# Performance work log

Hardware: AMD Instinct MI355X
Metric: run time of the kernel (lower is better)

## Reference

```python
import jax, jax.numpy as jnp
import numpy as np

B, S, E, D, H = 4, 2048, 512, 64, 8
NEG = float(np.finfo(np.float64).min)  # tf uses tf.float64.min; overflows to -inf in fp32, same softmax effect


def setup_inputs() -> dict:
    key = jax.random.key(0)
    ks = jax.random.split(key, 6)
    std = 0.05  # tf.random_normal_initializer default stddev
    x = jax.random.normal(ks[0], (B, S, E), dtype=jnp.float32)
    Wq = jax.random.normal(ks[1], (H, E, D), dtype=jnp.float32) * std
    Wk = jax.random.normal(ks[2], (H, E, D), dtype=jnp.float32) * std
    Wvd = jax.random.normal(ks[3], (H, E, D), dtype=jnp.float32) * std
    Wvu = jax.random.normal(ks[4], (H, D, E), dtype=jnp.float32) * std
    Wo = jax.random.normal(ks[5], (H, 1), dtype=jnp.float32) * std
    return {"x": x, "Wq": Wq, "Wk": Wk, "Wvd": Wvd, "Wvu": Wvu, "Wo": Wo}


def reference(x, Wq, Wk, Wvd, Wvu, Wo):
    # Per-head projections, vectorized over the head axis h
    Q = jnp.einsum("bse,hed->bhsd", x, Wq)  # [B,H,S,D]
    K = jnp.einsum("bse,hed->bhsd", x, Wk)
    score = jnp.einsum("bhsd,bhtd->bhst", Q, K) / jnp.sqrt(jnp.float32(D))
    # tf.linalg.band_part(score, -1, 0): keep lower triangle (causal)
    tril = jnp.tril(jnp.ones((S, S), dtype=bool))
    score = jnp.where(tril, score, 0.0)
    # tf.where(score != 0, score, float64.min): masks zeros (incl. any exact-zero kept entries)
    score = jnp.where(score != 0, score, jnp.float32(NEG))
    attn = jax.nn.softmax(score, axis=-1)  # [B,H,S,S]
    # low-rank value projection: x @ (Wvdown @ Wvup) per head
    Wv = jnp.einsum("hed,hdf->hef", Wvd, Wvu)  # [H,E,E]
    V = jnp.einsum("bse,hef->bhsf", x, Wv)      # [B,H,S,E]
    heads = jnp.einsum("bhst,bhte->bhse", attn, V)  # [B,H,S,E]
    # stack on last axis then matmul with Wo[H,1] == weighted sum over heads
    out = jnp.einsum("bhse,h->bse", heads, Wo[:, 0])
    return out
```

## Files before the change

kernel.cpp:

```cpp
#include <hip/hip_runtime.h>
#include <math.h>

namespace {
constexpr int B = 4, S = 2048, E = 512, D = 64, H = 8;
constexpr int KD = 512;

typedef short bf8 __attribute__((ext_vector_type(8)));
typedef short bf4 __attribute__((ext_vector_type(4)));
typedef float f4 __attribute__((ext_vector_type(4)));

__device__ __forceinline__ short f2bf(float f) {
  union { float f; unsigned u; } v; v.f = f;
  const unsigned r = v.u + 0x7fffu + ((v.u >> 16) & 1u);
  return (short)(r >> 16);
}

__device__ __forceinline__ unsigned cvt_pk_bf16(float a, float b) {
  unsigned r;
  asm("v_cvt_pk_bf16_f32 %0, %1, %2" : "=v"(r) : "v"(a), "v"(b));
  return r;
}

__device__ __forceinline__ void gload16(const void* g, void* l) {
  __builtin_amdgcn_global_load_lds(
      (const __attribute__((address_space(1))) unsigned int*)g,
      (__attribute__((address_space(3))) unsigned int*)l, 16, 0, 0);
}

__global__ __launch_bounds__(256) void xb_kernel(const float* __restrict__ x,
                                                 short* __restrict__ xb) {
  const size_t i = ((size_t)blockIdx.x * 256 + threadIdx.x) * 8;
  const float4 v0 = *(const float4*)(x + i);
  const float4 v1 = *(const float4*)(x + i + 4);
  bf8 o;
  o[0] = f2bf(v0.x); o[1] = f2bf(v0.y); o[2] = f2bf(v0.z); o[3] = f2bf(v0.w);
  o[4] = f2bf(v1.x); o[5] = f2bf(v1.y); o[6] = f2bf(v1.z); o[7] = f2bf(v1.w);
  *(bf8*)(xb + i) = o;
}

__global__ __launch_bounds__(256) void wcat_kernel(
    const float* __restrict__ Wq, const float* __restrict__ Wk,
    const float* __restrict__ Wvd, short* __restrict__ WcatT) {
  const int cb = blockIdx.x;
  const int e0 = blockIdx.y * 64;
  const int w = cb >> 3, h = cb & 7;
  const float* Wsel = (w == 0) ? Wq : (w == 1) ? Wk : Wvd;
  const float* Wp = Wsel + (size_t)h * E * D;
  __shared__ float T[64][65];
  const int tid = threadIdx.x;
#pragma unroll
  for (int i = 0; i < 4; ++i) {
    const int f = tid + i * 256;
    const int r = f >> 4, c4 = f & 15;
    const float4 v = *(const float4*)(Wp + (size_t)(e0 + r) * D + c4 * 4);
    T[r][c4 * 4 + 0] = v.x; T[r][c4 * 4 + 1] = v.y;
    T[r][c4 * 4 + 2] = v.z; T[r][c4 * 4 + 3] = v.w;
  }
  __syncthreads();
#pragma unroll
  for (int i = 0; i < 4; ++i) {
    const int f = tid + i * 256;
    const int dr = f >> 4, e4 = f & 15;
    bf4 o;
#pragma unroll
    for (int j = 0; j < 4; ++j) o[j] = f2bf(T[e4 * 4 + j][dr]);
    *(bf4*)(WcatT + (size_t)(cb * 64 + dr) * KD + e0 + e4 * 4) = o;
  }
}

__global__ __launch_bounds__(256) void w2t_kernel(
    const float* __restrict__ Wvu, const float* __restrict__ Wo,
    short* __restrict__ W2T) {
  const int h = blockIdx.x;
  const int e0 = blockIdx.y * 64;
  const float wo = Wo[h];
  __shared__ float T[64][65];
  const int tid = threadIdx.x;
#pragma unroll
  for (int i = 0; i < 4; ++i) {
    const int f = tid + i * 256;
    const int r = f >> 4, c4 = f & 15;
    const float4 v = *(const float4*)(Wvu + ((size_t)h * D + r) * E + e0 + c4 * 4);
    T[r][c4 * 4 + 0] = v.x * wo; T[r][c4 * 4 + 1] = v.y * wo;
    T[r][c4 * 4 + 2] = v.z * wo; T[r][c4 * 4 + 3] = v.w * wo;
  }
  __syncthreads();
#pragma unroll
  for (int i = 0; i < 4; ++i) {
    const int f = tid + i * 256;
    const int er = f >> 4, d4 = f & 15;
    bf4 o;
#pragma unroll
    for (int j = 0; j < 4; ++j) o[j] = f2bf(T[d4 * 4 + j][er]);
    *(bf4*)(W2T + (size_t)(e0 + er) * KD + h * 64 + d4 * 4) = o;
  }
}

template <int MODE>
__global__ __launch_bounds__(256) void gemm_kernel(
    const short* __restrict__ A, const short* __restrict__ Bt,
    short* __restrict__ Qb, short* __restrict__ Kb, short* __restrict__ Vtg,
    float* __restrict__ Of) {
  const int row0 = blockIdx.x * 128;
  const int ct = blockIdx.y;
  const int tid = threadIdx.x;
  const int w = tid >> 6, l = tid & 63;
  const int wm = w >> 1, wn = w & 1;
  const int lr = l & 15, hi = l >> 4;

  __shared__ short As[128 * 64];
  __shared__ short Bs[128 * 64];

  const short* Ag = A + (size_t)row0 * KD;
  const short* Bg = Bt + (size_t)ct * 128 * KD;

  f4 acc[4][4] = {};
  for (int k0 = 0; k0 < KD; k0 += 64) {
    __syncthreads();
#pragma unroll
    for (int i = 0; i < 4; ++i) {
      const int f = i * 256 + tid;
      const int r = f >> 3, g = f & 7;
      gload16(Ag + (size_t)r * KD + k0 + ((g ^ (r & 7)) << 3), &As[f * 8]);
    }
#pragma unroll
    for (int i = 0; i < 4; ++i) {
      const int f = i * 256 + tid;
      const int r = f >> 3, g = f & 7;
      gload16(Bg + (size_t)r * KD + k0 + ((g ^ (r & 7)) << 3), &Bs[f * 8]);
    }
    __syncthreads();

    bf8 af[4][2], bfv[4][2];
#pragma unroll
    for (int t = 0; t < 4; ++t) {
#pragma unroll
      for (int kh = 0; kh < 2; ++kh) {
        const int ar = wm * 64 + t * 16 + lr;
        af[t][kh] = *(const bf8*)&As[ar * 64 + (((kh * 4 + hi) ^ (ar & 7)) << 3)];
        const int br = wn * 64 + t * 16 + lr;
        bfv[t][kh] = *(const bf8*)&Bs[br * 64 + (((kh * 4 + hi) ^ (br & 7)) << 3)];
      }
    }
#pragma unroll
    for (int mt = 0; mt < 4; ++mt)
#pragma unroll
      for (int nt = 0; nt < 4; ++nt) {
        acc[mt][nt] =
            __builtin_amdgcn_mfma_f32_16x16x32_bf16(af[mt][0], bfv[nt][0], acc[mt][nt], 0, 0, 0);
        acc[mt][nt] =
            __builtin_amdgcn_mfma_f32_16x16x32_bf16(af[mt][1], bfv[nt][1], acc[mt][nt], 0, 0, 0);
      }
  }

  if constexpr (MODE == 0) {
#pragma unroll
    for (int nt = 0; nt < 4; ++nt) {
      const int gc = ct * 128 + wn * 64 + nt * 16 + lr;
      const int cb = gc >> 6, d = gc & 63;
      const int h = cb & 7;
      if (cb < 16) {
        short* Out = (cb < 8) ? Qb : Kb;
#pragma unroll
        for (int mt = 0; mt < 4; ++mt)
#pragma unroll
          for (int reg = 0; reg < 4; ++reg) {
            const int grow = row0 + wm * 64 + mt * 16 + hi * 4 + reg;
            const int b = grow >> 11, s = grow & (S - 1);
            Out[(((size_t)(b * H + h) * S + s) << 6) + d] = f2bf(acc[mt][nt][reg]);
          }
      } else {
#pragma unroll
        for (int mt = 0; mt < 4; ++mt) {
          const int grow0 = row0 + wm * 64 + mt * 16 + hi * 4;
          const int b = grow0 >> 11, s0 = grow0 & (S - 1);
          bf4 o;
#pragma unroll
          for (int reg = 0; reg < 4; ++reg) o[reg] = f2bf(acc[mt][nt][reg]);
          *(bf4*)(Vtg + (((size_t)(b * H + h) * D + d) << 11) + s0) = o;
        }
      }
    }
  } else {
#pragma unroll
    for (int mt = 0; mt < 4; ++mt)
#pragma unroll
      for (int reg = 0; reg < 4; ++reg) {
        const int grow = row0 + wm * 64 + mt * 16 + hi * 4 + reg;
        float* orow = Of + (size_t)grow * 512 + ct * 128 + wn * 64;
#pragma unroll
        for (int nt = 0; nt < 4; ++nt) orow[nt * 16 + lr] = acc[mt][nt][reg];
      }
  }
}

__global__ __launch_bounds__(256) void attn_kernel(
    const short* __restrict__ Qb, const short* __restrict__ Kb,
    const short* __restrict__ Vt, short* __restrict__ PVb) {
  const int bh = blockIdx.x;
  const int qt = (int)(gridDim.y - 1 - blockIdx.y);
  const int b = bh >> 3, h = bh & 7;
  const int tid = threadIdx.x;
  const int w = tid >> 6, l = tid & 63;
  const int lr = l & 15, hi = l >> 4;

  __shared__ short Ks[2][64 * 64];
  __shared__ short Vs[2][64 * 64];
  __shared__ short Ps[4][16 * 64];

  const short* Qg = Qb + ((size_t)bh * S + qt * 64 + w * 16 + lr) * D;
  const bf8 qf0 = *(const bf8*)(Qg + hi * 8);
  const bf8 qf1 = *(const bf8*)(Qg + 32 + hi * 8);

  const short* Kg = Kb + (size_t)bh * S * D;
  const short* Vg = Vt + (size_t)bh * D * S;

  const int sr = tid >> 3, sg = tid & 7;
  const int sswz = (sg ^ (sr & 7)) << 3;
  const int sr2 = sr + 32, sswz2 = (sg ^ (sr2 & 7)) << 3;

  float lsum = 0.f;
  f4 accO[4] = {};

  constexpr float LOG2E = 1.44269504088896340736f;
  constexpr float C1 = 0.125f * LOG2E;
  constexpr float C0 = -12.0f * LOG2E;

  short* Pw = Ps[w];
  const int c7 = lr & 7;

  gload16(Kg + (size_t)sr * D + sswz, &Ks[0][tid * 8]);
  gload16(Kg + (size_t)sr2 * D + sswz2, &Ks[0][(256 + tid) * 8]);
  gload16(Vg + (size_t)sr * S + sswz, &Vs[0][tid * 8]);
  gload16(Vg + (size_t)sr2 * S + sswz2, &Vs[0][(256 + tid) * 8]);
  __syncthreads();

  auto step = [&](const short* Kl, const short* Vl, auto diag_c) {
    constexpr bool DIAG = decltype(diag_c)::value;
    f4 accS[4] = {};
    __builtin_amdgcn_s_setprio(1);
#pragma unroll
    for (int n = 0; n < 4; ++n) {
      const int tr = n * 16 + lr;
      const bf8 k0 = *(const bf8*)&Kl[tr * 64 + ((hi ^ (tr & 7)) << 3)];
      const bf8 k1 = *(const bf8*)&Kl[tr * 64 + (((4 + hi) ^ (tr & 7)) << 3)];
      accS[n] = __builtin_amdgcn_mfma_f32_16x16x32_bf16(k0, qf0, accS[n], 0, 0, 0);
      accS[n] = __builtin_amdgcn_mfma_f32_16x16x32_bf16(k1, qf1, accS[n], 0, 0, 0);
    }
    __builtin_amdgcn_s_setprio(0);

#pragma unroll
    for (int n = 0; n < 4; ++n) {
      float p[4];
#pragma unroll
      for (int reg = 0; reg < 4; ++reg) {
        const float sv = accS[n][reg];
        bool ok = (sv != 0.f);
        if constexpr (DIAG) ok = ok && (n * 16 + hi * 4 + reg <= w * 16 + lr);
        p[reg] = ok ? exp2f(fmaf(sv, C1, C0)) : 0.f;
        lsum += p[reg];
      }
      int2 pk;
      pk.x = (int)cvt_pk_bf16(p[0], p[1]);
      pk.y = (int)cvt_pk_bf16(p[2], p[3]);
      const int gi = 2 * n + (hi >> 1);
      *(int2*)&Pw[lr * 64 + ((gi ^ c7) << 3) + (hi & 1) * 4] = pk;
    }

    __builtin_amdgcn_s_setprio(1);
#pragma unroll
    for (int kh = 0; kh < 2; ++kh) {
      const bf8 pf = *(const bf8*)&Pw[lr * 64 + (((kh * 4 + hi) ^ c7) << 3)];
#pragma unroll
      for (int n = 0; n < 4; ++n) {
        const int er = n * 16 + lr;
        const bf8 vf = *(const bf8*)&Vl[er * 64 + (((kh * 4 + hi) ^ (er & 7)) << 3)];
        accO[n] = __builtin_amdgcn_mfma_f32_16x16x32_bf16(pf, vf, accO[n], 0, 0, 0);
      }
    }
    __builtin_amdgcn_s_setprio(0);
  };

  int buf = 0;
  for (int kt = 0; kt <= qt; ++kt) {
    if (kt < qt) {
      const int nb = buf ^ 1;
      const size_t koff = (size_t)(kt + 1) * 64;
      gload16(Kg + (koff + sr) * D + sswz, &Ks[nb][tid * 8]);
      gload16(Kg + (koff + sr2) * D + sswz2, &Ks[nb][(256 + tid) * 8]);
      gload16(Vg + (size_t)sr * S + koff + sswz, &Vs[nb][tid * 8]);
      gload16(Vg + (size_t)sr2 * S + koff + sswz2, &Vs[nb][(256 + tid) * 8]);
    }
    if (kt < qt) {
      step(Ks[buf], Vs[buf], std::integral_constant<bool, false>{});
    } else {
      step(Ks[buf], Vs[buf], std::integral_constant<bool, true>{});
    }
    __syncthreads();
    buf ^= 1;
  }

  float lv = lsum;
  lv += __shfl_xor(lv, 16);
  lv += __shfl_xor(lv, 32);
#pragma unroll
  for (int reg = 0; reg < 4; ++reg) {
    const float lq = __shfl(lv, hi * 4 + reg);
    const float inv = 1.f / lq;
    const int s = qt * 64 + w * 16 + hi * 4 + reg;
    short* op = PVb + (size_t)(b * S + s) * (H * D) + h * D;
#pragma unroll
    for (int n = 0; n < 4; ++n) op[n * 16 + lr] = f2bf(accO[n][reg] * inv);
  }
}

}

extern "C" void kernel_launch(void* const* d_in, const int* in_sizes, int n_in,
                              void* d_out, int out_size, void* d_ws, size_t ws_size,
                              hipStream_t stream) {
  const float* x   = (const float*)d_in[0];
  const float* Wq  = (const float*)d_in[1];
  const float* Wk  = (const float*)d_in[2];
  const float* Wvd = (const float*)d_in[3];
  const float* Wvu = (const float*)d_in[4];
  const float* Wo  = (const float*)d_in[5];
  float* out = (float*)d_out;

  const size_t nqk = (size_t)B * H * S * D;
  short* xb    = (short*)d_ws;
  short* Qb    = xb + nqk;
  short* Kb    = Qb + nqk;
  short* Vtg   = Kb + nqk;
  short* PVb   = Vtg + nqk;
  short* WcatT = PVb + nqk;
  short* W2T   = WcatT + 1536 * KD;

  xb_kernel<<<dim3(B * S * E / (256 * 8)), 256, 0, stream>>>(x, xb);
  wcat_kernel<<<dim3(24, 8), 256, 0, stream>>>(Wq, Wk, Wvd, WcatT);
  w2t_kernel<<<dim3(8, 8), 256, 0, stream>>>(Wvu, Wo, W2T);
  gemm_kernel<0><<<dim3(64, 12), 256, 0, stream>>>(xb, WcatT, Qb, Kb, Vtg, nullptr);
  attn_kernel<<<dim3(B * H, S / 64), 256, 0, stream>>>(Qb, Kb, Vtg, PVb);
  gemm_kernel<1><<<dim3(64, 4), 256, 0, stream>>>(PVb, W2T, nullptr, nullptr, nullptr, out);
}
```

Measured before the change: 94.04 us.

## Merge prep kernels and restructure attention K/V double-buffer sync

Combines the three preprocessing kernels (x to bf16, weight concat-transpose, Wvu*Wo transpose) into one launch, with block ranges selecting the role. This cuts per-launch overhead. In attention, the trailing __syncthreads is replaced by explicit s_barrier plus s_waitcnt vmcnt(4), so the next tile's prefetch stays in flight while the current tile is computed, and pointers are advanced incrementally. The hand-written waitcnt relies on the compiler's count of outstanding loads and could break correctness if that count differs.

```diff
diff --git a/kernel.cpp b/kernel.cpp
--- a/kernel.cpp
+++ b/kernel.cpp
@@ -1,5 +1,6 @@
 #include <hip/hip_runtime.h>
 #include <math.h>
+#include <type_traits>
 
 namespace {
 constexpr int B = 4, S = 2048, E = 512, D = 64, H = 8;
@@ -27,72 +28,69 @@
       (__attribute__((address_space(3))) unsigned int*)l, 16, 0, 0);
 }
 
-__global__ __launch_bounds__(256) void xb_kernel(const float* __restrict__ x,
-                                                 short* __restrict__ xb) {
-  const size_t i = ((size_t)blockIdx.x * 256 + threadIdx.x) * 8;
-  const float4 v0 = *(const float4*)(x + i);
-  const float4 v1 = *(const float4*)(x + i + 4);
-  bf8 o;
-  o[0] = f2bf(v0.x); o[1] = f2bf(v0.y); o[2] = f2bf(v0.z); o[3] = f2bf(v0.w);
-  o[4] = f2bf(v1.x); o[5] = f2bf(v1.y); o[6] = f2bf(v1.z); o[7] = f2bf(v1.w);
-  *(bf8*)(xb + i) = o;
-}
-
-__global__ __launch_bounds__(256) void wcat_kernel(
-    const float* __restrict__ Wq, const float* __restrict__ Wk,
-    const float* __restrict__ Wvd, short* __restrict__ WcatT) {
-  const int cb = blockIdx.x;
-  const int e0 = blockIdx.y * 64;
-  const int w = cb >> 3, h = cb & 7;
-  const float* Wsel = (w == 0) ? Wq : (w == 1) ? Wk : Wvd;
-  const float* Wp = Wsel + (size_t)h * E * D;
+__global__ __launch_bounds__(256) void prep_kernel(
+    const float* __restrict__ x, const float* __restrict__ Wq,
+    const float* __restrict__ Wk, const float* __restrict__ Wvd,
+    const float* __restrict__ Wvu, const float* __restrict__ Wo,
+    short* __restrict__ xb, short* __restrict__ WcatT,
+    short* __restrict__ W2T) {
   __shared__ float T[64][65];
+  const int bid = blockIdx.x;
   const int tid = threadIdx.x;
-#pragma unroll
-  for (int i = 0; i < 4; ++i) {
-    const int f = tid + i * 256;
-    const int r = f >> 4, c4 = f & 15;
-    const float4 v = *(const float4*)(Wp + (size_t)(e0 + r) * D + c4 * 4);
-    T[r][c4 * 4 + 0] = v.x; T[r][c4 * 4 + 1] = v.y;
-    T[r][c4 * 4 + 2] = v.z; T[r][c4 * 4 + 3] = v.w;
-  }
-  __syncthreads();
-#pragma unroll
-  for (int i = 0; i < 4; ++i) {
-    const int f = tid + i * 256;
-    const int dr = f >> 4, e4 = f & 15;
-    bf4 o;
-#pragma unroll
-    for (int j = 0; j < 4; ++j) o[j] = f2bf(T[e4 * 4 + j][dr]);
-    *(bf4*)(WcatT + (size_t)(cb * 64 + dr) * KD + e0 + e4 * 4) = o;
-  }
-}
-
-__global__ __launch_bounds__(256) void w2t_kernel(
-    const float* __restrict__ Wvu, const float* __restrict__ Wo,
-    short* __restrict__ W2T) {
-  const int h = blockIdx.x;
-  const int e0 = blockIdx.y * 64;
-  const float wo = Wo[h];
-  __shared__ float T[64][65];
-  const int tid = threadIdx.x;
-#pragma unroll
-  for (int i = 0; i < 4; ++i) {
-    const int f = tid + i * 256;
-    const int r = f >> 4, c4 = f & 15;
-    const float4 v = *(const float4*)(Wvu + ((size_t)h * D + r) * E + e0 + c4 * 4);
-    T[r][c4 * 4 + 0] = v.x * wo; T[r][c4 * 4 + 1] = v.y * wo;
-    T[r][c4 * 4 + 2] = v.z * wo; T[r][c4 * 4 + 3] = v.w * wo;
-  }
-  __syncthreads();
-#pragma unroll
-  for (int i = 0; i < 4; ++i) {
-    const int f = tid + i * 256;
-    const int er = f >> 4, d4 = f & 15;
-    bf4 o;
-#pragma unroll
-    for (int j = 0; j < 4; ++j) o[j] = f2bf(T[d4 * 4 + j][er]);
-    *(bf4*)(W2T + (size_t)(e0 + er) * KD + h * 64 + d4 * 4) = o;
+  if (bid < 2048) {
+    const size_t i = ((size_t)bid * 256 + tid) * 8;
+    const float4 v0 = *(const float4*)(x + i);
+    const float4 v1 = *(const float4*)(x + i + 4);
+    bf8 o;
+    o[0] = f2bf(v0.x); o[1] = f2bf(v0.y); o[2] = f2bf(v0.z); o[3] = f2bf(v0.w);
+    o[4] = f2bf(v1.x); o[5] = f2bf(v1.y); o[6] = f2bf(v1.z); o[7] = f2bf(v1.w);
+    *(bf8*)(xb + i) = o;
+  } else if (bid < 2240) {
+    const int r = bid - 2048;
+    const int cb = r >> 3, e0 = (r & 7) * 64;
+    const int w = cb >> 3, h = cb & 7;
+    const float* Wsel = (w == 0) ? Wq : (w == 1) ? Wk : Wvd;
+    const float* Wp = Wsel + (size_t)h * E * D;
+#pragma unroll
+    for (int i = 0; i < 4; ++i) {
+      const int f = tid + i * 256;
+      const int rr = f >> 4, c4 = f & 15;
+      const float4 v = *(const float4*)(Wp + (size_t)(e0 + rr) * D + c4 * 4);
+      T[rr][c4 * 4 + 0] = v.x; T[rr][c4 * 4 + 1] = v.y;
+      T[rr][c4 * 4 + 2] = v.z; T[rr][c4 * 4 + 3] = v.w;
+    }
+    __syncthreads();
+#pragma unroll
+    for (int i = 0; i < 4; ++i) {
+      const int f = tid + i * 256;
+      const int dr = f >> 4, e4 = f & 15;
+      bf4 o;
+#pragma unroll
+      for (int j = 0; j < 4; ++j) o[j] = f2bf(T[e4 * 4 + j][dr]);
+      *(bf4*)(WcatT + (size_t)(cb * 64 + dr) * KD + e0 + e4 * 4) = o;
+    }
+  } else {
+    const int r = bid - 2240;
+    const int h = r >> 3, e0 = (r & 7) * 64;
+    const float wo = Wo[h];
+#pragma unroll
+    for (int i = 0; i < 4; ++i) {
+      const int f = tid + i * 256;
+      const int rr = f >> 4, c4 = f & 15;
+      const float4 v = *(const float4*)(Wvu + ((size_t)h * D + rr) * E + e0 + c4 * 4);
+      T[rr][c4 * 4 + 0] = v.x * wo; T[rr][c4 * 4 + 1] = v.y * wo;
+      T[rr][c4 * 4 + 2] = v.z * wo; T[rr][c4 * 4 + 3] = v.w * wo;
+    }
+    __syncthreads();
+#pragma unroll
+    for (int i = 0; i < 4; ++i) {
+      const int f = tid + i * 256;
+      const int er = f >> 4, d4 = f & 15;
+      bf4 o;
+#pragma unroll
+      for (int j = 0; j < 4; ++j) o[j] = f2bf(T[d4 * 4 + j][er]);
+      *(bf4*)(W2T + (size_t)(e0 + er) * KD + h * 64 + d4 * 4) = o;
+    }
   }
 }
 
@@ -204,8 +202,10 @@
   const int w = tid >> 6, l = tid & 63;
   const int lr = l & 15, hi = l >> 4;
 
-  __shared__ short Ks[2][64 * 64];
-  __shared__ short Vs[2][64 * 64];
+  __shared__ short KsA[64 * 64];
+  __shared__ short KsB[64 * 64];
+  __shared__ short VsA[64 * 64];
+  __shared__ short VsB[64 * 64];
   __shared__ short Ps[4][16 * 64];
 
   const short* Qg = Qb + ((size_t)bh * S + qt * 64 + w * 16 + lr) * D;
@@ -219,6 +219,11 @@
   const int sswz = (sg ^ (sr & 7)) << 3;
   const int sr2 = sr + 32, sswz2 = (sg ^ (sr2 & 7)) << 3;
 
+  const short* kg0 = Kg + (size_t)sr * D + sswz;
+  const short* kg1 = Kg + (size_t)sr2 * D + sswz2;
+  const short* vg0 = Vg + (size_t)sr * S + sswz;
+  const short* vg1 = Vg + (size_t)sr2 * S + sswz2;
+
   float lsum = 0.f;
   f4 accO[4] = {};
 
@@ -228,12 +233,6 @@
 
   short* Pw = Ps[w];
   const int c7 = lr & 7;
-
-  gload16(Kg + (size_t)sr * D + sswz, &Ks[0][tid * 8]);
-  gload16(Kg + (size_t)sr2 * D + sswz2, &Ks[0][(256 + tid) * 8]);
-  gload16(Vg + (size_t)sr * S + sswz, &Vs[0][tid * 8]);
-  gload16(Vg + (size_t)sr2 * S + sswz2, &Vs[0][(256 + tid) * 8]);
-  __syncthreads();
 
   auto step = [&](const short* Kl, const short* Vl, auto diag_c) {
     constexpr bool DIAG = decltype(diag_c)::value;
@@ -281,23 +280,40 @@
     __builtin_amdgcn_s_setprio(0);
   };
 
-  int buf = 0;
+  gload16(kg0, &KsA[tid * 8]);
+  gload16(kg1, &KsA[(256 + tid) * 8]);
+  gload16(vg0, &VsA[tid * 8]);
+  gload16(vg1, &VsA[(256 + tid) * 8]);
+  kg0 += 64 * D; kg1 += 64 * D; vg0 += 64; vg1 += 64;
+
+  short* Kc = KsA; short* Vc = VsA;
+  short* Kn = KsB; short* Vn = VsB;
+
   for (int kt = 0; kt <= qt; ++kt) {
+    if (kt > 0) {
+      __builtin_amdgcn_s_barrier();
+      __builtin_amdgcn_sched_barrier(0);
+    }
     if (kt < qt) {
-      const int nb = buf ^ 1;
-      const size_t koff = (size_t)(kt + 1) * 64;
-      gload16(Kg + (koff + sr) * D + sswz, &Ks[nb][tid * 8]);
-      gload16(Kg + (koff + sr2) * D + sswz2, &Ks[nb][(256 + tid) * 8]);
-      gload16(Vg + (size_t)sr * S + koff + sswz, &Vs[nb][tid * 8]);
-      gload16(Vg + (size_t)sr2 * S + koff + sswz2, &Vs[nb][(256 + tid) * 8]);
-    }
+      gload16(kg0, &Kn[tid * 8]);
+      gload16(kg1, &Kn[(256 + tid) * 8]);
+      gload16(vg0, &Vn[tid * 8]);
+      gload16(vg1, &Vn[(256 + tid) * 8]);
+      kg0 += 64 * D; kg1 += 64 * D; vg0 += 64; vg1 += 64;
+      asm volatile("s_waitcnt vmcnt(4)" ::: "memory");
+    } else {
+      asm volatile("s_waitcnt vmcnt(0)" ::: "memory");
+    }
+    __builtin_amdgcn_sched_barrier(0);
+    __builtin_amdgcn_s_barrier();
+    __builtin_amdgcn_sched_barrier(0);
+
     if (kt < qt) {
-      step(Ks[buf], Vs[buf], std::integral_constant<bool, false>{});
+      step(Kc, Vc, std::integral_constant<bool, false>{});
     } else {
-      step(Ks[buf], Vs[buf], std::integral_constant<bool, true>{});
-    }
-    __syncthreads();
-    buf ^= 1;
+      step(Kc, Vc, std::integral_constant<bool, true>{});
+    }
+    { short* t = Kc; Kc = Kn; Kn = t; t = Vc; Vc = Vn; Vn = t; }
   }
 
   float lv = lsum;
@@ -336,9 +352,8 @@
   short* WcatT = PVb + nqk;
   short* W2T   = WcatT + 1536 * KD;
 
-  xb_kernel<<<dim3(B * S * E / (256 * 8)), 256, 0, stream>>>(x, xb);
-  wcat_kernel<<<dim3(24, 8), 256, 0, stream>>>(Wq, Wk, Wvd, WcatT);
-  w2t_kernel<<<dim3(8, 8), 256, 0, stream>>>(Wvu, Wo, W2T);
+  prep_kernel<<<dim3(2304), 256, 0, stream>>>(x, Wq, Wk, Wvd, Wvu, Wo,
+                                              xb, WcatT, W2T);
   gemm_kernel<0><<<dim3(64, 12), 256, 0, stream>>>(xb, WcatT, Qb, Kb, Vtg, nullptr);
   attn_kernel<<<dim3(B * H, S / 64), 256, 0, stream>>>(Qb, Kb, Vtg, PVb);
   gemm_kernel<1><<<dim3(64, 4), 256, 0, stream>>>(PVb, W2T, nullptr, nullptr, nullptr, out);
```

After: 85.62 us. 9.0% less time.
